# Kernel optimization log

Hardware: AMD Instinct MI355X
Metric: run time of the kernel (lower is better)

The kernel has to match this reference:

```python
import jax, jax.numpy as jnp
import numpy as np

N, E, F, B = 50000, 100000, 80000, 64   # nodes, edges, faces, graphs
S, T, D = 32, 32, 3                      # bump_steps, num_thetas, num_features
R = 1.1
SHARP = 500.0                            # sigmoid sharpness from the source


def setup_inputs() -> dict:
    key = jax.random.key(0)
    k = jax.random.split(key, 6)
    x = jax.random.normal(k[0], (N, D), dtype=jnp.float32)
    node_weights = jax.random.uniform(k[1], (N,), dtype=jnp.float32)
    v = jax.random.uniform(k[2], (D, T), dtype=jnp.float32) - 0.5  # Parameter init: rand - 0.5
    lin = jnp.linspace(-R, R, S).astype(jnp.float32)               # bump thresholds
    edge_index = jax.random.randint(k[3], (2, E), 0, N)
    face = jax.random.randint(k[4], (3, F), 0, N)
    batch = jnp.sort(jax.random.randint(k[5], (N,), 0, B))         # sorted graph ids per node
    return {"x": x, "node_weights": node_weights, "v": v, "lin": lin,
            "edge_index": edge_index, "face": face, "batch": batch}


def _wecc(h, index, lin, weight):
    # h: [M, T] heights, index: [M] graph ids, weight: [M]
    # ecc: [M, S, T] = sigmoid(500*(lin - h)) * weight, then scatter-add by graph.
    ecc = jax.nn.sigmoid(SHARP * (lin[None, :, None] - h[:, None, :])) * weight[:, None, None]
    # segment_sum over simplices == index_add on dim 1 followed by movedim(0,1) -> [B, S, T]
    return jax.ops.segment_sum(ecc, index, num_segments=B)


def reference(x, node_weights, v, lin, edge_index, face, batch):
    nh = x @ v                                   # [N, T] node heights
    eh = jnp.min(nh[edge_index], axis=0)         # [E, T] edge height = min of endpoints
    fh = jnp.min(nh[face], axis=0)               # [F, T] face height = min of vertices
    edge_w = jnp.max(node_weights[edge_index], axis=0)  # [E]
    face_w = jnp.max(node_weights[face], axis=0)        # [F]
    out = _wecc(nh, batch, lin, node_weights)
    out = out - _wecc(eh, batch[edge_index[0]], lin, edge_w)
    out = out + _wecc(fh, batch[face[0]], lin, face_w)
    return out  # [B, S, T]
```

## Files before the change

### kernel.cpp

```cpp
#include <hip/hip_runtime.h>

#define NB      64
#define SS      32
#define TT      32
#define RADIUSF 1.1f
#define NC      16
#define NROWS   34
#define NCNT    128
#define BCAP    1440
#define UCAP    4096

__global__ __launch_bounds__(256) void k_init(
    const int* __restrict__ batch, int* __restrict__ cur,
    int* __restrict__ ns, int Nn)
{
    const int tid = threadIdx.x;
    if (tid < NB) cur[tid] = 0;
    if (tid <= NB) {
        int lo = 0, hi = Nn;
        while (lo < hi) { const int mid = (lo + hi) >> 1; if (batch[mid] < tid) lo = mid + 1; else hi = mid; }
        ns[tid] = lo;
    }
}

__global__ __launch_bounds__(256) void k_build(
    const float* __restrict__ nw, const int* __restrict__ ei,
    const int* __restrict__ fc, const int* __restrict__ batch,
    int* __restrict__ cur, int4* __restrict__ U, int E, int F)
{
    __shared__ int lc[NB];
    __shared__ int lb[NB];
    __shared__ int   r_i0[BCAP], r_i1[BCAP], r_i2[BCAP];
    __shared__ float r_w[BCAP];
    __shared__ unsigned char r_b[BCAP];
    const int tid = threadIdx.x;
    const int EF = E + F;

    if (tid < NB) lc[tid] = 0;
    __syncthreads();

    const int j0 = (int)((long long)EF * blockIdx.x / NCNT);
    const int j1 = (int)((long long)EF * (blockIdx.x + 1) / NCNT);
    for (int j = j0 + tid, idx = tid; j < j1; j += 256, idx += 256) {
        int i0, i1, i2; float w;
        if (j < E) {
            i0 = ei[j]; i1 = ei[E + j]; i2 = i0;
            w = -fmaxf(nw[i0], nw[i1]);
        } else {
            const int f = j - E;
            i0 = fc[f]; i1 = fc[F + f]; i2 = fc[2 * F + f];
            w = fmaxf(nw[i0], fmaxf(nw[i1], nw[i2]));
        }
        const int b = batch[i0];
        r_i0[idx] = i0; r_i1[idx] = i1; r_i2[idx] = i2;
        r_w[idx] = w; r_b[idx] = (unsigned char)b;
        atomicAdd(&lc[b], 1);
    }
    __syncthreads();
    if (tid < NB) { const int c = lc[tid]; lb[tid] = c ? atomicAdd(&cur[tid], c) : 0; lc[tid] = 0; }
    __syncthreads();
    const int cnt = j1 - j0;
    for (int idx = tid; idx < cnt; idx += 256) {
        const int b = r_b[idx];
        const int r = atomicAdd(&lc[b], 1);
        U[(b << 12) + lb[b] + r] =
            make_int4(r_i0[idx], r_i1[idx], r_i2[idx], __float_as_int(r_w[idx]));
    }
}

__global__ __launch_bounds__(256) void k_main2(
    const float* __restrict__ x, const float* __restrict__ nw,
    const float* __restrict__ v, const int4* __restrict__ U,
    const int* __restrict__ ns, const int* __restrict__ cur,
    float* __restrict__ partial)
{
    __shared__ float hist[4][NROWS * 64];

    const int tid  = threadIdx.x;
    const int wave = tid >> 6;
    const int lane = tid & 63;
    const int t    = lane & 31;
    const int half = lane >> 5;
    const int b     = blockIdx.x & 63;
    const int chunk = blockIdx.x >> 6;

    float* H = hist[wave];
    for (int i = tid; i < 4 * NROWS * 64; i += 256) ((float*)hist)[i] = 0.0f;
    __syncthreads();

    const float v0 = v[t], v1 = v[TT + t], v2 = v[2 * TT + t];

    const float INV = 31.0f / 2.2f;
    const float DLT = 2.2f / 31.0f;

#define BODY(hv, wv)                                                        \
    {                                                                       \
        const float hr = hv + RADIUSF;                                      \
        float sf = rintf(hr * INV);                                         \
        sf = fminf(fmaxf(sf, 0.0f), 32.0f);                                 \
        const float t1 = __builtin_fmaf(sf, -DLT, hr);                      \
        const float Ee = __expf(500.0f * t1);                               \
        const float sg = __builtin_amdgcn_rcpf(1.0f + Ee);                  \
        const float dA = wv * sg;                                           \
        const float dB = wv - dA;                                           \
        float* p = H + (int)sf * 64 + lane;                                 \
        p[0]  += dA;                                                        \
        p[64] += dB;                                                        \
    }

    {
        const int g0 = ns[b], g1 = ns[b + 1];
        const int gc = g1 - g0;
        const int m0 = g0 + (int)(((long long)gc * chunk) / NC);
        const int m1 = g0 + (int)(((long long)gc * (chunk + 1)) / NC);
        for (int k = m0 + wave * 2; k < m1; k += 8) {
            const int n = min(k + half, m1 - 1);
            const float x0 = x[3 * n], x1 = x[3 * n + 1], x2 = x[3 * n + 2];
            const float h = __builtin_fmaf(x0, v0, __builtin_fmaf(x1, v1, x2 * v2));
            const float w = nw[n];
            if (k + half < m1) BODY(h, w)
        }
    }

    {
        const int g0 = b << 12;
        const int gc = min(cur[b], UCAP);
        const int m0 = g0 + (int)(((long long)gc * chunk) / NC);
        const int m1 = g0 + (int)(((long long)gc * (chunk + 1)) / NC);
        int k = m0 + wave * 2;
        if (k < m1) {
            int4 q = U[min(k + half, m1 - 1)];
            while (k < m1) {
                const int kn = k + 8;
                const int4 qn = U[min(kn + half, m1 - 1)];
                const float a0 = x[3 * q.x], a1 = x[3 * q.x + 1], a2 = x[3 * q.x + 2];
                const float b0 = x[3 * q.y], b1 = x[3 * q.y + 1], b2 = x[3 * q.y + 2];
                const float c0 = x[3 * q.z], c1 = x[3 * q.z + 1], c2 = x[3 * q.z + 2];
                const float h0 = __builtin_fmaf(a0, v0, __builtin_fmaf(a1, v1, a2 * v2));
                const float h1 = __builtin_fmaf(b0, v0, __builtin_fmaf(b1, v1, b2 * v2));
                const float h2 = __builtin_fmaf(c0, v0, __builtin_fmaf(c1, v1, c2 * v2));
                const float h = fminf(h0, fminf(h1, h2));
                const float w = __int_as_float(q.w);
                if (k + half < m1) BODY(h, w)
                q = qn;
                k = kn;
            }
        }
    }
#undef BODY

    __syncthreads();
    float* dst = partial + ((size_t)blockIdx.x << 10);
    for (int i = tid; i < SS * TT; i += 256) {
        const int s = i >> 5, t2 = i & 31;
        float acc = 0.0f;
#pragma unroll
        for (int wv = 0; wv < 4; ++wv)
            acc += hist[wv][s * 64 + t2] + hist[wv][s * 64 + t2 + 32];
        dst[i] = acc;
    }
}

__global__ __launch_bounds__(1024) void k_finish(
    const float* __restrict__ partial, float* __restrict__ out)
{
    __shared__ float tile[SS * TT];
    const int b   = blockIdx.x;
    const int tid = threadIdx.x;
    float acc = 0.0f;
#pragma unroll
    for (int c = 0; c < NC; ++c) acc += partial[(((size_t)(c * NB + b)) << 10) + tid];
    tile[tid] = acc;
    __syncthreads();
    const int t = tid & 31, s = tid >> 5;
    float run = 0.0f;
    for (int sp = 0; sp <= s; ++sp) run += tile[(sp << 5) + t];
    out[((size_t)b << 10) + tid] = run;
}

extern "C" void kernel_launch(void* const* d_in, const int* in_sizes, int n_in,
                              void* d_out, int out_size, void* d_ws, size_t ws_size,
                              hipStream_t stream)
{
    const float* x     = (const float*)d_in[0];
    const float* nw    = (const float*)d_in[1];
    const float* v     = (const float*)d_in[2];
    const int*   ei    = (const int*)d_in[4];
    const int*   fc    = (const int*)d_in[5];
    const int*   batch = (const int*)d_in[6];
    float*       out   = (float*)d_out;

    const int Nn = in_sizes[1];
    const int E  = in_sizes[4] / 2;
    const int F  = in_sizes[5] / 3;

    auto align256 = [](size_t v_) { return (v_ + 255) & ~(size_t)255; };
    const size_t U_b    = align256((size_t)NB * UCAP * sizeof(int4));
    const size_t part_b = align256((size_t)NC * NB * SS * TT * sizeof(float));

    int4*  U       = (int4*)d_ws;
    float* partial = (float*)((char*)d_ws + U_b);
    int*   cur     = (int*)((char*)d_ws + U_b + part_b);
    int*   ns      = cur + 64;

    k_init <<<1, 256, 0, stream>>>(batch, cur, ns, Nn);
    k_build<<<NCNT, 256, 0, stream>>>(nw, ei, fc, batch, cur, U, E, F);
    k_main2<<<NC * NB, 256, 0, stream>>>(x, nw, v, U, ns, cur, partial);
    k_finish<<<NB, 1024, 0, stream>>>(partial, out);
}
```

Baseline: 37.41 us.

## Pre-gather vertex coordinates into bucketed records and pack node data as float4

```diff
diff --git a/kernel.cpp b/kernel.cpp
--- a/kernel.cpp
+++ b/kernel.cpp
@@ -7,6 +7,7 @@
 #define NC      16
 #define NROWS   34
 #define NCNT    128
+#define NRB     64
 #define BCAP    1440
 #define UCAP    4096
 
@@ -24,16 +25,28 @@
 }
 
 __global__ __launch_bounds__(256) void k_build(
-    const float* __restrict__ nw, const int* __restrict__ ei,
-    const int* __restrict__ fc, const int* __restrict__ batch,
-    int* __restrict__ cur, int4* __restrict__ U, int E, int F)
-{
+    const float* __restrict__ x, const float* __restrict__ nw,
+    const int* __restrict__ ei, const int* __restrict__ fc,
+    const int* __restrict__ batch, int* __restrict__ cur,
+    float4* __restrict__ Urec, float4* __restrict__ NR,
+    int Nn, int E, int F)
+{
+    const int tid = threadIdx.x;
+
+    if ((int)blockIdx.x >= NCNT) {
+        const int blk = blockIdx.x - NCNT;
+        const int n0 = (int)((long long)Nn * blk / NRB);
+        const int n1 = (int)((long long)Nn * (blk + 1) / NRB);
+        for (int n = n0 + tid; n < n1; n += 256)
+            NR[n] = make_float4(x[3 * n], x[3 * n + 1], x[3 * n + 2], nw[n]);
+        return;
+    }
+
     __shared__ int lc[NB];
     __shared__ int lb[NB];
     __shared__ int   r_i0[BCAP], r_i1[BCAP], r_i2[BCAP];
     __shared__ float r_w[BCAP];
     __shared__ unsigned char r_b[BCAP];
-    const int tid = threadIdx.x;
     const int EF = E + F;
 
     if (tid < NB) lc[tid] = 0;
@@ -63,16 +76,19 @@
     for (int idx = tid; idx < cnt; idx += 256) {
         const int b = r_b[idx];
         const int r = atomicAdd(&lc[b], 1);
-        U[(b << 12) + lb[b] + r] =
-            make_int4(r_i0[idx], r_i1[idx], r_i2[idx], __float_as_int(r_w[idx]));
+        const int slot = (b << 12) + lb[b] + r;
+        const int i0 = r_i0[idx], i1 = r_i1[idx], i2 = r_i2[idx];
+        float4* dst = Urec + (size_t)slot * 3;
+        dst[0] = make_float4(x[3 * i0], x[3 * i0 + 1], x[3 * i0 + 2], r_w[idx]);
+        dst[1] = make_float4(x[3 * i1], x[3 * i1 + 1], x[3 * i1 + 2], 0.0f);
+        dst[2] = make_float4(x[3 * i2], x[3 * i2 + 1], x[3 * i2 + 2], 0.0f);
     }
 }
 
 __global__ __launch_bounds__(256) void k_main2(
-    const float* __restrict__ x, const float* __restrict__ nw,
-    const float* __restrict__ v, const int4* __restrict__ U,
-    const int* __restrict__ ns, const int* __restrict__ cur,
-    float* __restrict__ partial)
+    const float4* __restrict__ NR, const float* __restrict__ v,
+    const float4* __restrict__ Urec, const int* __restrict__ ns,
+    const int* __restrict__ cur, float* __restrict__ partial)
 {
     __shared__ float hist[4][NROWS * 64];
 
@@ -115,10 +131,9 @@
         const int m1 = g0 + (int)(((long long)gc * (chunk + 1)) / NC);
         for (int k = m0 + wave * 2; k < m1; k += 8) {
             const int n = min(k + half, m1 - 1);
-            const float x0 = x[3 * n], x1 = x[3 * n + 1], x2 = x[3 * n + 2];
-            const float h = __builtin_fmaf(x0, v0, __builtin_fmaf(x1, v1, x2 * v2));
-            const float w = nw[n];
-            if (k + half < m1) BODY(h, w)
+            const float4 r = NR[n];
+            const float h = __builtin_fmaf(r.x, v0, __builtin_fmaf(r.y, v1, r.z * v2));
+            if (k + half < m1) BODY(h, r.w)
         }
     }
 
@@ -129,20 +144,18 @@
         const int m1 = g0 + (int)(((long long)gc * (chunk + 1)) / NC);
         int k = m0 + wave * 2;
         if (k < m1) {
-            int4 q = U[min(k + half, m1 - 1)];
+            const float4* rec = Urec + (size_t)min(k + half, m1 - 1) * 3;
+            float4 A = rec[0], Bv = rec[1], Cv = rec[2];
             while (k < m1) {
                 const int kn = k + 8;
-                const int4 qn = U[min(kn + half, m1 - 1)];
-                const float a0 = x[3 * q.x], a1 = x[3 * q.x + 1], a2 = x[3 * q.x + 2];
-                const float b0 = x[3 * q.y], b1 = x[3 * q.y + 1], b2 = x[3 * q.y + 2];
-                const float c0 = x[3 * q.z], c1 = x[3 * q.z + 1], c2 = x[3 * q.z + 2];
-                const float h0 = __builtin_fmaf(a0, v0, __builtin_fmaf(a1, v1, a2 * v2));
-                const float h1 = __builtin_fmaf(b0, v0, __builtin_fmaf(b1, v1, b2 * v2));
-                const float h2 = __builtin_fmaf(c0, v0, __builtin_fmaf(c1, v1, c2 * v2));
+                const float4* recn = Urec + (size_t)min(kn + half, m1 - 1) * 3;
+                const float4 An = recn[0], Bn = recn[1], Cn = recn[2];
+                const float h0 = __builtin_fmaf(A.x,  v0, __builtin_fmaf(A.y,  v1, A.z  * v2));
+                const float h1 = __builtin_fmaf(Bv.x, v0, __builtin_fmaf(Bv.y, v1, Bv.z * v2));
+                const float h2 = __builtin_fmaf(Cv.x, v0, __builtin_fmaf(Cv.y, v1, Cv.z * v2));
                 const float h = fminf(h0, fminf(h1, h2));
-                const float w = __int_as_float(q.w);
-                if (k + half < m1) BODY(h, w)
-                q = qn;
+                if (k + half < m1) BODY(h, A.w)
+                A = An; Bv = Bn; Cv = Cn;
                 k = kn;
             }
         }
@@ -195,16 +208,18 @@
     const int F  = in_sizes[5] / 3;
 
     auto align256 = [](size_t v_) { return (v_ + 255) & ~(size_t)255; };
-    const size_t U_b    = align256((size_t)NB * UCAP * sizeof(int4));
+    const size_t U_b    = align256((size_t)NB * UCAP * 48);
     const size_t part_b = align256((size_t)NC * NB * SS * TT * sizeof(float));
-
-    int4*  U       = (int4*)d_ws;
-    float* partial = (float*)((char*)d_ws + U_b);
-    int*   cur     = (int*)((char*)d_ws + U_b + part_b);
-    int*   ns      = cur + 64;
+    const size_t NR_b   = align256((size_t)Nn * sizeof(float4));
+
+    float4* Urec    = (float4*)d_ws;
+    float*  partial = (float*)((char*)d_ws + U_b);
+    float4* NR      = (float4*)((char*)d_ws + U_b + part_b);
+    int*    cur     = (int*)((char*)d_ws + U_b + part_b + NR_b);
+    int*    ns      = cur + 64;
 
     k_init <<<1, 256, 0, stream>>>(batch, cur, ns, Nn);
-    k_build<<<NCNT, 256, 0, stream>>>(nw, ei, fc, batch, cur, U, E, F);
-    k_main2<<<NC * NB, 256, 0, stream>>>(x, nw, v, U, ns, cur, partial);
+    k_build<<<NCNT + NRB, 256, 0, stream>>>(x, nw, ei, fc, batch, cur, Urec, NR, Nn, E, F);
+    k_main2<<<NC * NB, 256, 0, stream>>>(NR, v, Urec, ns, cur, partial);
     k_finish<<<NB, 1024, 0, stream>>>(partial, out);
 }
```

Measured after the change: 42.34 us. +13.2%, slower.
